# Optimization experiments

Hardware: AMD Instinct MI355X
Metric: run time of the kernel (lower is better)

The kernel has to match this reference:

```python
import jax, jax.numpy as jnp
import numpy as np

B, D, N, K = 4, 256, 4096, 8192


def setup_inputs() -> dict:
    key = jax.random.key(0)
    kx, ke = jax.random.split(key)
    x = jax.random.normal(kx, (B, D, N), dtype=jnp.float32)
    e = jax.random.normal(ke, (K, D), dtype=jnp.float32)
    return {"x": x, "e": e}


def reference(x, e):
    # encode: cdist(x^T [B,N,D], e [K,D]) -> [B,N,K]; argmin over K.
    # sqrt is monotonic, so argmin of squared distance == argmin of cdist.
    xt = jnp.transpose(x, (0, 2, 1))                      # [B,N,D]
    x2 = jnp.sum(xt * xt, axis=-1, keepdims=True)         # [B,N,1]
    e2 = jnp.sum(e * e, axis=-1)                          # [K]
    d2 = x2 - 2.0 * jnp.einsum('bnd,kd->bnk', xt, e) + e2 # [B,N,K]
    codes = jnp.argmin(d2, axis=-1)                       # [B,N]
    # decode: embedding gather then transpose back to [B,D,N]
    quantized = e[codes]                                  # [B,N,D]
    return jnp.transpose(quantized, (0, 2, 1))            # [B,D,N]
```

## Files before the change

kernel.cpp:

```cpp
#include <hip/hip_runtime.h>
#include <stdint.h>

#define B_ 4
#define D_ 256
#define N_ 4096
#define K_ 8192
#define Q_ (B_*N_)

typedef __attribute__((ext_vector_type(8))) short bf16x8;
typedef __attribute__((ext_vector_type(8))) unsigned short u16x8;
typedef __attribute__((ext_vector_type(16))) float f32x16;

__device__ __forceinline__ unsigned short f32_to_bf16(float f) {
  unsigned u = __float_as_uint(f);
  unsigned r = 0x7FFFu + ((u >> 16) & 1u);
  return (unsigned short)((u + r) >> 16);
}
__device__ __forceinline__ float bf16_to_f32(unsigned short h) {
  return __uint_as_float(((unsigned)h) << 16);
}

__device__ __forceinline__ void gl_lds16(const void* g, void* l) {
  __builtin_amdgcn_global_load_lds(
      (const __attribute__((address_space(1))) unsigned int*)g,
      (__attribute__((address_space(3))) unsigned int*)l, 16, 0, 0);
}

__global__ void prep_x_kernel(const float* __restrict__ x,
                              unsigned short* __restrict__ xh,
                              unsigned short* __restrict__ xl) {
  __shared__ float tile[64][65];
  int b = blockIdx.z;
  int d0 = blockIdx.y * 64;
  int n0 = blockIdx.x * 64;
  int tid = threadIdx.x;

  int rr = tid >> 4;
  int rc = (tid & 15) * 4;
  const float* xp = x + ((size_t)b * D_ + d0) * N_ + n0;
#pragma unroll
  for (int p = 0; p < 4; ++p) {
    float4 v = *(const float4*)(xp + (size_t)(rr + 16 * p) * N_ + rc);
    tile[rr + 16 * p][rc + 0] = v.x;
    tile[rr + 16 * p][rc + 1] = v.y;
    tile[rr + 16 * p][rc + 2] = v.z;
    tile[rr + 16 * p][rc + 3] = v.w;
  }
  __syncthreads();

  int nr = tid >> 3;
  int dc = tid & 7;
#pragma unroll
  for (int p = 0; p < 2; ++p) {
    int nn = nr + 32 * p;
    u16x8 h8, l8;
#pragma unroll
    for (int j = 0; j < 8; ++j) {
      float v = tile[dc * 8 + j][nn];
      unsigned short h = f32_to_bf16(v);
      h8[j] = h;
      l8[j] = f32_to_bf16(v - bf16_to_f32(h));
    }
    size_t q = (size_t)b * N_ + n0 + nn;
    *(u16x8*)(xh + q * D_ + d0 + dc * 8) = h8;
    *(u16x8*)(xl + q * D_ + d0 + dc * 8) = l8;
  }
}

__global__ void prep_e_kernel(const float* __restrict__ e,
                              unsigned short* __restrict__ eh,
                              unsigned short* __restrict__ el,
                              float* __restrict__ e2h,
                              unsigned long long* __restrict__ keys) {
  int tid = threadIdx.x;
  int k = blockIdx.x * 8 + (tid >> 5);
  int d = (tid & 31) * 8;
  if (tid < 16) keys[(size_t)blockIdx.x * 16 + tid] = ~0ull;
  const float* ep = e + (size_t)k * D_ + d;
  float4 v0 = *(const float4*)(ep);
  float4 v1 = *(const float4*)(ep + 4);
  float vv[8] = {v0.x, v0.y, v0.z, v0.w, v1.x, v1.y, v1.z, v1.w};
  u16x8 h8, l8;
  float s = 0.f;
#pragma unroll
  for (int j = 0; j < 8; ++j) {
    unsigned short h = f32_to_bf16(vv[j]);
    h8[j] = h;
    l8[j] = f32_to_bf16(vv[j] - bf16_to_f32(h));
    s += vv[j] * vv[j];
  }
  *(u16x8*)(eh + (size_t)k * D_ + d) = h8;
  *(u16x8*)(el + (size_t)k * D_ + d) = l8;
#pragma unroll
  for (int off = 16; off > 0; off >>= 1) s += __shfl_xor(s, off, 64);
  if ((tid & 31) == 0) e2h[k] = 0.5f * s;
}

__global__ __launch_bounds__(256, 2) void vq_main_kernel(
    const unsigned short* __restrict__ xh, const unsigned short* __restrict__ xl,
    const unsigned short* __restrict__ eh, const unsigned short* __restrict__ el,
    const float* __restrict__ e2h, unsigned long long* __restrict__ keys) {
  __shared__ __attribute__((aligned(16))) unsigned short Bs[2][2][32 * 256];

  const int tid = threadIdx.x;
  const int w = tid >> 6;
  const int lane = tid & 63;
  const int l = lane & 31;
  const int hi = lane >> 5;

  const int qt = blockIdx.x >> 2;
  const int ks4 = blockIdx.x & 3;
  const int q0 = qt * 128;
  const int kbase = ks4 * 2048;
  const int qw = q0 + w * 32;

  bf16x8 ah[16], al[16];
  {
    const unsigned short* pa = xh + (size_t)(qw + l) * D_ + hi * 8;
    const unsigned short* pb = xl + (size_t)(qw + l) * D_ + hi * 8;
#pragma unroll
    for (int kc16 = 0; kc16 < 16; ++kc16) {
      ah[kc16] = *(const bf16x8*)(pa + kc16 * 16);
      al[kc16] = *(const bf16x8*)(pb + kc16 * 16);
    }
  }

  float rminv[16];
  int rmini[16];
#pragma unroll
  for (int r = 0; r < 16; ++r) { rminv[r] = __builtin_inff(); rmini[r] = 0; }

  auto stage = [&](int ch, int buf) {
    const int kc = kbase + ch * 32;
#pragma unroll
    for (int p = 0; p < 4; ++p) {
      const int c0 = w * 8 + p * 2;
      const int c = c0 + hi;
      const int g = l ^ (c & 31);
      const size_t srcoff = (size_t)(kc + c) * D_ + g * 8;
      gl_lds16(eh + srcoff, &Bs[buf][0][c0 * 256]);
      gl_lds16(el + srcoff, &Bs[buf][1][c0 * 256]);
    }
  };

  stage(0, 0);

#pragma unroll 1
  for (int ch = 0; ch < 64; ++ch) {
    const int buf = ch & 1;
    __syncthreads();
    if (ch + 1 < 64) stage(ch + 1, buf ^ 1);
    const int kc = kbase + ch * 32;
    const float e2v = e2h[kc + l];

    f32x16 acc;
#pragma unroll
    for (int r = 0; r < 16; ++r) acc[r] = 0.f;

#pragma unroll
    for (int ks = 0; ks < 16; ++ks) {
      const int pos = (((ks * 2 + hi) ^ l) * 8);
      bf16x8 bh = *(const bf16x8*)&Bs[buf][0][l * 256 + pos];
      bf16x8 bl = *(const bf16x8*)&Bs[buf][1][l * 256 + pos];
      acc = __builtin_amdgcn_mfma_f32_32x32x16_bf16(ah[ks], bh, acc, 0, 0, 0);
      acc = __builtin_amdgcn_mfma_f32_32x32x16_bf16(ah[ks], bl, acc, 0, 0, 0);
      acc = __builtin_amdgcn_mfma_f32_32x32x16_bf16(al[ks], bh, acc, 0, 0, 0);
    }

    const int kidx = kc + l;
#pragma unroll
    for (int r = 0; r < 16; ++r) {
      float dv = e2v - acc[r];
      bool better = dv < rminv[r];
      rminv[r] = better ? dv : rminv[r];
      rmini[r] = better ? kidx : rmini[r];
    }
  }

#pragma unroll
  for (int r = 0; r < 16; ++r) {
    float bv = rminv[r];
    int bi = rmini[r];
#pragma unroll
    for (int xm = 1; xm <= 16; xm <<= 1) {
      float ov = __shfl_xor(bv, xm, 64);
      int oi = __shfl_xor(bi, xm, 64);
      if (ov < bv || (ov == bv && oi < bi)) { bv = ov; bi = oi; }
    }
    if (l == 0) {
      const int m = (r & 3) + 8 * (r >> 2) + 4 * hi;
      const int qq = qw + m;
      unsigned su = __float_as_uint(bv);
      su ^= (unsigned)(((int)su >> 31) | 0x80000000u);
      unsigned long long key = ((unsigned long long)su << 32) | (unsigned)bi;
      atomicMin(keys + qq, key);
    }
  }
}

__global__ void decode_kernel(const unsigned long long* __restrict__ keys,
                              const float* __restrict__ e,
                              float* __restrict__ out) {
  size_t gid = (size_t)blockIdx.x * 256 + threadIdx.x;
  int nq = (int)(gid % (N_ / 4));
  int rest = (int)(gid / (N_ / 4));
  int d = rest % D_;
  int b = rest / D_;
  int n0 = nq * 4;
  const unsigned long long* kp = keys + (size_t)b * N_ + n0;
  float4 o;
  o.x = e[(size_t)(unsigned)(kp[0] & 0xFFFFFFFFull) * D_ + d];
  o.y = e[(size_t)(unsigned)(kp[1] & 0xFFFFFFFFull) * D_ + d];
  o.z = e[(size_t)(unsigned)(kp[2] & 0xFFFFFFFFull) * D_ + d];
  o.w = e[(size_t)(unsigned)(kp[3] & 0xFFFFFFFFull) * D_ + d];
  *(float4*)(out + ((size_t)b * D_ + d) * N_ + n0) = o;
}

extern "C" void kernel_launch(void* const* d_in, const int* in_sizes, int n_in,
                              void* d_out, int out_size, void* d_ws, size_t ws_size,
                              hipStream_t stream) {
  const float* x = (const float*)d_in[0];
  const float* e = (const float*)d_in[1];
  float* out = (float*)d_out;

  char* wksp = (char*)d_ws;
  unsigned short* xh = (unsigned short*)wksp;
  unsigned short* xl = xh + (size_t)Q_ * D_;
  unsigned short* eh = xl + (size_t)Q_ * D_;
  unsigned short* el = eh + (size_t)K_ * D_;
  float* e2h = (float*)(el + (size_t)K_ * D_);
  unsigned long long* keys = (unsigned long long*)(e2h + K_);

  prep_x_kernel<<<dim3(N_ / 64, D_ / 64, B_), 256, 0, stream>>>(x, xh, xl);
  prep_e_kernel<<<K_ / 8, 256, 0, stream>>>(e, eh, el, e2h, keys);
  vq_main_kernel<<<512, 256, 0, stream>>>(xh, xl, eh, el, e2h, keys);
  decode_kernel<<<(Q_ * D_) / 1024, 256, 0, stream>>>(keys, e, out);
}
```

Before: 269.5 us.

## Double per-wave query tile in VQ main kernel and stage decode via LDS

Each wave now computes two 32-row query blocks against every staged codebook chunk, so each LDS B-fragment load feeds twice as many MFMAs and block count halves to 256. Launch bounds drop to one block per SU to fit the doubled A fragments and accumulators in registers. Decode is rewritten to gather whole codebook rows coalesced into an LDS tile and write the transposed output from there, replacing strided per-element gathers. The risks are lower occupancy and only 256 blocks on a 256-CU GPU, which leaves little latency hiding.

```diff
diff --git a/kernel.cpp b/kernel.cpp
--- a/kernel.cpp
+++ b/kernel.cpp
@@ -96,7 +96,7 @@
   if ((tid & 31) == 0) e2h[k] = 0.5f * s;
 }
 
-__global__ __launch_bounds__(256, 2) void vq_main_kernel(
+__global__ __launch_bounds__(256, 1) void vq_main_kernel(
     const unsigned short* __restrict__ xh, const unsigned short* __restrict__ xl,
     const unsigned short* __restrict__ eh, const unsigned short* __restrict__ el,
     const float* __restrict__ e2h, unsigned long long* __restrict__ keys) {
@@ -110,25 +110,28 @@
 
   const int qt = blockIdx.x >> 2;
   const int ks4 = blockIdx.x & 3;
-  const int q0 = qt * 128;
+  const int q0 = qt * 256;
   const int kbase = ks4 * 2048;
-  const int qw = q0 + w * 32;
-
-  bf16x8 ah[16], al[16];
-  {
-    const unsigned short* pa = xh + (size_t)(qw + l) * D_ + hi * 8;
-    const unsigned short* pb = xl + (size_t)(qw + l) * D_ + hi * 8;
-#pragma unroll
-    for (int kc16 = 0; kc16 < 16; ++kc16) {
-      ah[kc16] = *(const bf16x8*)(pa + kc16 * 16);
-      al[kc16] = *(const bf16x8*)(pb + kc16 * 16);
-    }
-  }
-
-  float rminv[16];
-  int rmini[16];
-#pragma unroll
-  for (int r = 0; r < 16; ++r) { rminv[r] = __builtin_inff(); rmini[r] = 0; }
+  const int qw = q0 + w * 64;
+
+  bf16x8 ah[2][16], al[2][16];
+#pragma unroll
+  for (int mb = 0; mb < 2; ++mb) {
+    const unsigned short* pa = xh + (size_t)(qw + mb * 32 + l) * D_ + hi * 8;
+    const unsigned short* pb = xl + (size_t)(qw + mb * 32 + l) * D_ + hi * 8;
+#pragma unroll
+    for (int k16 = 0; k16 < 16; ++k16) {
+      ah[mb][k16] = *(const bf16x8*)(pa + k16 * 16);
+      al[mb][k16] = *(const bf16x8*)(pb + k16 * 16);
+    }
+  }
+
+  float rminv[2][16];
+  int rmini[2][16];
+#pragma unroll
+  for (int mb = 0; mb < 2; ++mb)
+#pragma unroll
+    for (int r = 0; r < 16; ++r) { rminv[mb][r] = __builtin_inff(); rmini[mb][r] = 0; }
 
   auto stage = [&](int ch, int buf) {
     const int kc = kbase + ch * 32;
@@ -153,67 +156,90 @@
     const int kc = kbase + ch * 32;
     const float e2v = e2h[kc + l];
 
-    f32x16 acc;
-#pragma unroll
-    for (int r = 0; r < 16; ++r) acc[r] = 0.f;
+    f32x16 acc0, acc1;
+#pragma unroll
+    for (int r = 0; r < 16; ++r) { acc0[r] = 0.f; acc1[r] = 0.f; }
 
 #pragma unroll
     for (int ks = 0; ks < 16; ++ks) {
       const int pos = (((ks * 2 + hi) ^ l) * 8);
       bf16x8 bh = *(const bf16x8*)&Bs[buf][0][l * 256 + pos];
       bf16x8 bl = *(const bf16x8*)&Bs[buf][1][l * 256 + pos];
-      acc = __builtin_amdgcn_mfma_f32_32x32x16_bf16(ah[ks], bh, acc, 0, 0, 0);
-      acc = __builtin_amdgcn_mfma_f32_32x32x16_bf16(ah[ks], bl, acc, 0, 0, 0);
-      acc = __builtin_amdgcn_mfma_f32_32x32x16_bf16(al[ks], bh, acc, 0, 0, 0);
+      acc0 = __builtin_amdgcn_mfma_f32_32x32x16_bf16(ah[0][ks], bh, acc0, 0, 0, 0);
+      acc1 = __builtin_amdgcn_mfma_f32_32x32x16_bf16(ah[1][ks], bh, acc1, 0, 0, 0);
+      acc0 = __builtin_amdgcn_mfma_f32_32x32x16_bf16(ah[0][ks], bl, acc0, 0, 0, 0);
+      acc1 = __builtin_amdgcn_mfma_f32_32x32x16_bf16(ah[1][ks], bl, acc1, 0, 0, 0);
+      acc0 = __builtin_amdgcn_mfma_f32_32x32x16_bf16(al[0][ks], bh, acc0, 0, 0, 0);
+      acc1 = __builtin_amdgcn_mfma_f32_32x32x16_bf16(al[1][ks], bh, acc1, 0, 0, 0);
     }
 
     const int kidx = kc + l;
 #pragma unroll
     for (int r = 0; r < 16; ++r) {
-      float dv = e2v - acc[r];
-      bool better = dv < rminv[r];
-      rminv[r] = better ? dv : rminv[r];
-      rmini[r] = better ? kidx : rmini[r];
-    }
-  }
-
-#pragma unroll
-  for (int r = 0; r < 16; ++r) {
-    float bv = rminv[r];
-    int bi = rmini[r];
-#pragma unroll
-    for (int xm = 1; xm <= 16; xm <<= 1) {
-      float ov = __shfl_xor(bv, xm, 64);
-      int oi = __shfl_xor(bi, xm, 64);
-      if (ov < bv || (ov == bv && oi < bi)) { bv = ov; bi = oi; }
-    }
-    if (l == 0) {
-      const int m = (r & 3) + 8 * (r >> 2) + 4 * hi;
-      const int qq = qw + m;
-      unsigned su = __float_as_uint(bv);
-      su ^= (unsigned)(((int)su >> 31) | 0x80000000u);
-      unsigned long long key = ((unsigned long long)su << 32) | (unsigned)bi;
-      atomicMin(keys + qq, key);
-    }
-  }
-}
-
-__global__ void decode_kernel(const unsigned long long* __restrict__ keys,
-                              const float* __restrict__ e,
-                              float* __restrict__ out) {
-  size_t gid = (size_t)blockIdx.x * 256 + threadIdx.x;
-  int nq = (int)(gid % (N_ / 4));
-  int rest = (int)(gid / (N_ / 4));
-  int d = rest % D_;
-  int b = rest / D_;
-  int n0 = nq * 4;
-  const unsigned long long* kp = keys + (size_t)b * N_ + n0;
-  float4 o;
-  o.x = e[(size_t)(unsigned)(kp[0] & 0xFFFFFFFFull) * D_ + d];
-  o.y = e[(size_t)(unsigned)(kp[1] & 0xFFFFFFFFull) * D_ + d];
-  o.z = e[(size_t)(unsigned)(kp[2] & 0xFFFFFFFFull) * D_ + d];
-  o.w = e[(size_t)(unsigned)(kp[3] & 0xFFFFFFFFull) * D_ + d];
-  *(float4*)(out + ((size_t)b * D_ + d) * N_ + n0) = o;
+      float dv0 = e2v - acc0[r];
+      bool b0 = dv0 < rminv[0][r];
+      rminv[0][r] = b0 ? dv0 : rminv[0][r];
+      rmini[0][r] = b0 ? kidx : rmini[0][r];
+      float dv1 = e2v - acc1[r];
+      bool b1 = dv1 < rminv[1][r];
+      rminv[1][r] = b1 ? dv1 : rminv[1][r];
+      rmini[1][r] = b1 ? kidx : rmini[1][r];
+    }
+  }
+
+#pragma unroll
+  for (int mb = 0; mb < 2; ++mb) {
+#pragma unroll
+    for (int r = 0; r < 16; ++r) {
+      float bv = rminv[mb][r];
+      int bi = rmini[mb][r];
+#pragma unroll
+      for (int xm = 1; xm <= 16; xm <<= 1) {
+        float ov = __shfl_xor(bv, xm, 64);
+        int oi = __shfl_xor(bi, xm, 64);
+        if (ov < bv || (ov == bv && oi < bi)) { bv = ov; bi = oi; }
+      }
+      if (l == 0) {
+        const int m = (r & 3) + 8 * (r >> 2) + 4 * hi;
+        const int qq = qw + mb * 32 + m;
+        unsigned su = __float_as_uint(bv);
+        su ^= (unsigned)(((int)su >> 31) | 0x80000000u);
+        unsigned long long key = ((unsigned long long)su << 32) | (unsigned)bi;
+        atomicMin(keys + qq, key);
+      }
+    }
+  }
+}
+
+__global__ __launch_bounds__(256, 2) void decode_kernel(
+    const unsigned long long* __restrict__ keys,
+    const float* __restrict__ e, float* __restrict__ out) {
+  __shared__ float tile[64][257];
+  int b = blockIdx.x >> 6;
+  int n0 = (blockIdx.x & 63) * 64;
+  int tid = threadIdx.x;
+  int w = tid >> 6, lane = tid & 63;
+
+#pragma unroll
+  for (int j = 0; j < 16; ++j) {
+    int i = w * 16 + j;
+    unsigned idx = (unsigned)(keys[(size_t)b * N_ + n0 + i] & 0xFFFFFFFFull);
+    float4 v = *(const float4*)(e + (size_t)idx * D_ + lane * 4);
+    *(float4*)&tile[i][lane * 4] = v;
+  }
+  __syncthreads();
+
+  int nq = tid & 15, dr = tid >> 4;
+#pragma unroll
+  for (int p = 0; p < 16; ++p) {
+    int d = dr + p * 16;
+    float4 o;
+    o.x = tile[nq * 4 + 0][d];
+    o.y = tile[nq * 4 + 1][d];
+    o.z = tile[nq * 4 + 2][d];
+    o.w = tile[nq * 4 + 3][d];
+    *(float4*)(out + ((size_t)b * D_ + d) * N_ + n0 + nq * 4) = o;
+  }
 }
 
 extern "C" void kernel_launch(void* const* d_in, const int* in_sizes, int n_in,
@@ -233,6 +259,6 @@
 
   prep_x_kernel<<<dim3(N_ / 64, D_ / 64, B_), 256, 0, stream>>>(x, xh, xl);
   prep_e_kernel<<<K_ / 8, 256, 0, stream>>>(e, eh, el, e2h, keys);
-  vq_main_kernel<<<512, 256, 0, stream>>>(xh, xl, eh, el, e2h, keys);
-  decode_kernel<<<(Q_ * D_) / 1024, 256, 0, stream>>>(keys, e, out);
-}
+  vq_main_kernel<<<256, 256, 0, stream>>>(xh, xl, eh, el, e2h, keys);
+  decode_kernel<<<256, 256, 0, stream>>>(keys, e, out);
+}
```

After: 264.1 us. 2.0% less time.
